# Kernel optimization log

Hardware: AMD Instinct MI355X
Metric: run time of the kernel (lower is better)

The kernel has to match this reference:

```python
import jax, jax.numpy as jnp
import numpy as np

B, T, D, L, H = 32, 256, 1024, 2, 8
DH = D // H          # 128 head dim
HID = 256            # GRU hidden per direction (d_model >> 1)
WIN = 3              # attn_width
NEG = -1e10


def setup_inputs() -> dict:
    key = jax.random.key(0)
    ks = jax.random.split(key, 20)
    s = 0.02
    inp = {}
    inp["x"] = jax.random.normal(ks[0], (B, T, 2560), jnp.float32)
    inp["mask"] = jnp.ones((B, T), jnp.int32)
    # face-feature projection Linear(1536, 512)
    inp["W_tran"] = jax.random.normal(ks[1], (1536, 512), jnp.float32) * s
    inp["b_tran"] = jnp.zeros((512,), jnp.float32)
    # stacked MHA params, one slice per layer
    inp["Wq"] = jax.random.normal(ks[2], (L, D, D), jnp.float32) * s
    inp["bq"] = jnp.zeros((L, D), jnp.float32)
    inp["Wk"] = jax.random.normal(ks[3], (L, D, D), jnp.float32) * s
    inp["bk"] = jnp.zeros((L, D), jnp.float32)
    inp["Wv"] = jax.random.normal(ks[4], (L, D, D), jnp.float32) * s
    inp["bv"] = jnp.zeros((L, D), jnp.float32)
    inp["Wo"] = jax.random.normal(ks[5], (L, D, D), jnp.float32) * s
    inp["bo"] = jnp.zeros((L, D), jnp.float32)
    # bidirectional GRU params (torch layout: [3H, in], gates r,z,n)
    inp["W_ih_f"] = jax.random.normal(ks[6], (3 * HID, D), jnp.float32) * s
    inp["W_hh_f"] = jax.random.normal(ks[7], (3 * HID, HID), jnp.float32) * s
    inp["b_ih_f"] = jnp.zeros((3 * HID,), jnp.float32)
    inp["b_hh_f"] = jnp.zeros((3 * HID,), jnp.float32)
    inp["W_ih_b"] = jax.random.normal(ks[8], (3 * HID, D), jnp.float32) * s
    inp["W_hh_b"] = jax.random.normal(ks[9], (3 * HID, HID), jnp.float32) * s
    inp["b_ih_b"] = jnp.zeros((3 * HID,), jnp.float32)
    inp["b_hh_b"] = jnp.zeros((3 * HID,), jnp.float32)
    return inp


def _gru(xs, W_ih, W_hh, b_ih, b_hh):
    # xs: [T, B, D] -> ys: [T, B, HID]
    gx = jnp.einsum('tbd,gd->tbg', xs, W_ih) + b_ih  # [T,B,3H]

    def step(h, g):
        gh = jnp.einsum('bh,gh->bg', h, W_hh) + b_hh
        r = jax.nn.sigmoid(g[:, :HID] + gh[:, :HID])
        z = jax.nn.sigmoid(g[:, HID:2 * HID] + gh[:, HID:2 * HID])
        n = jnp.tanh(g[:, 2 * HID:] + r * gh[:, 2 * HID:])
        h_new = (1.0 - z) * n + z * h
        return h_new, h_new

    h0 = jnp.zeros((xs.shape[1], HID), xs.dtype)
    _, ys = jax.lax.scan(step, h0, gx)
    return ys


def reference(x, mask, W_tran, b_tran, Wq, bq, Wk, bk, Wv, bv, Wo, bo,
              W_ih_f, W_hh_f, b_ih_f, b_hh_f, W_ih_b, W_hh_b, b_ih_b, b_hh_b):
    # split feature streams (Movie101 branch)
    x_face = jnp.einsum('btf,fd->btd', x[:, :, 1024:], W_tran) + b_tran  # [B,T,512]
    h = x[:, :, :1024]                                                   # [B,T,1024]

    # banded self-attn mask: 0 within |i-j|<=3, else -1e10
    idx = jnp.arange(T)
    band = jnp.where(jnp.abs(idx[:, None] - idx[None, :]) <= WIN, 0.0, NEG).astype(h.dtype)

    scale = 1.0 / np.sqrt(DH)
    for l in range(L):
        res = h
        q = (jnp.einsum('btd,de->bte', h, Wq[l]) + bq[l]).reshape(B, T, H, DH)
        k = (jnp.einsum('btd,de->bte', h, Wk[l]) + bk[l]).reshape(B, T, H, DH)
        v = (jnp.einsum('btd,de->bte', h, Wv[l]) + bv[l]).reshape(B, T, H, DH)
        scores = jnp.einsum('bqhd,bkhd->bhqk', q, k) * scale + band  # [B,H,T,T]
        attn = jax.nn.softmax(scores, axis=-1)
        out = jnp.einsum('bhqk,bkhd->bqhd', attn, v).reshape(B, T, D)
        out = jnp.einsum('btd,de->bte', out, Wo[l]) + bo[l]
        h = res + out  # dropout is identity in eval mode

    # BiGRU over time, respecting per-sequence lengths (packed semantics)
    xs = jnp.transpose(h, (1, 0, 2))                      # [T,B,1024]
    lengths = mask.sum(axis=-1)                           # [B]
    t_idx = jnp.arange(T)[:, None]                        # [T,1]
    valid = (t_idx < lengths[None, :]).astype(h.dtype)    # [T,B]

    ys_f = _gru(xs, W_ih_f, W_hh_f, b_ih_f, b_hh_f) * valid[:, :, None]

    # reverse each sequence within its own length
    rev_idx = jnp.clip(lengths[None, :] - 1 - t_idx, 0)   # [T,B]
    xs_rev = jnp.take_along_axis(xs, rev_idx[:, :, None], axis=0)
    ys_b = _gru(xs_rev, W_ih_b, W_hh_b, b_ih_b, b_hh_b)
    ys_b = jnp.take_along_axis(ys_b, rev_idx[:, :, None], axis=0) * valid[:, :, None]

    rnn_out = jnp.concatenate([ys_f, ys_b], axis=-1)      # [T,B,512]
    out = jnp.transpose(rnn_out, (1, 0, 2))               # [B,T,512]
    return out + x_face
```

## Files before the change

kernel.cpp:

```cpp
#include <hip/hip_runtime.h>
#include <hip/hip_fp16.h>

#define B_   32
#define T_   256
#define D_   1024
#define H_   8
#define HID_ 256

typedef unsigned short u16;
typedef __attribute__((ext_vector_type(8))) short  s16x8;
typedef __attribute__((ext_vector_type(8))) __bf16 bf16x8;
typedef __attribute__((ext_vector_type(4))) float  f32x4;
typedef __attribute__((ext_vector_type(2))) _Float16 h2v;
typedef __attribute__((ext_vector_type(8))) _Float16 h8;

__device__ __forceinline__ u16 f2bf(float f){
  union { float f; unsigned u; } v; v.f = f;
  unsigned r = v.u + 0x7FFFu + ((v.u >> 16) & 1u);
  return (u16)(r >> 16);
}
__device__ __forceinline__ float bf2f(u16 u){
  union { unsigned u; float f; } v; v.u = ((unsigned)u) << 16; return v.f;
}

__device__ __forceinline__ f32x4 mfma_bf16(s16x8 a, s16x8 b, f32x4 c){
  bf16x8 av, bv;
  __builtin_memcpy(&av, &a, 16);
  __builtin_memcpy(&bv, &b, 16);
  return __builtin_amdgcn_mfma_f32_16x16x32_bf16(av, bv, c, 0, 0, 0);
}

__device__ __forceinline__ void gld16(const void* g, void* l){
  __builtin_amdgcn_global_load_lds((const __attribute__((address_space(1))) void*)g,
                                   (__attribute__((address_space(3))) void*)l, 16, 0, 0);
}

#if defined(__has_builtin)
#if __has_builtin(__builtin_amdgcn_fdot2)
#define HAVE_FDOT2 1
#endif
#endif

__device__ __forceinline__ float fdot2f(h2v a, h2v b, float c){
#ifdef HAVE_FDOT2
  return __builtin_amdgcn_fdot2(a, b, c, false);
#else
  return c + (float)a[0]*(float)b[0] + (float)a[1]*(float)b[1];
#endif
}

__global__ void k_conv_x(const float* __restrict__ x, u16* __restrict__ h,
                         u16* __restrict__ xfb){
  int m = blockIdx.x;
  int i = threadIdx.x * 8;
  const float4* p = (const float4*)(x + (size_t)m*2560 + i);
  float4 a = p[0], b = p[1];
  union { u16 u[8]; uint4 v; } o;
  o.u[0]=f2bf(a.x); o.u[1]=f2bf(a.y); o.u[2]=f2bf(a.z); o.u[3]=f2bf(a.w);
  o.u[4]=f2bf(b.x); o.u[5]=f2bf(b.y); o.u[6]=f2bf(b.z); o.u[7]=f2bf(b.w);
  u16* dst = (i < 1024) ? (h + (size_t)m*1024 + i) : (xfb + (size_t)m*1536 + (i-1024));
  *(uint4*)dst = o.v;
}

__global__ void k_transpose_bf16(const float* __restrict__ in, u16* __restrict__ out,
                                 int K, int N){
  __shared__ u16 tile[64][65];
  int kb = blockIdx.y * 64, nb = blockIdx.x * 64;
  int tid = threadIdx.x;
  {
    int k  = tid >> 2;
    int n0 = (tid & 3) * 16;
    const float* ip = in + (size_t)(kb + k) * N + nb + n0;
    #pragma unroll
    for (int i = 0; i < 4; ++i){
      float4 v = *(const float4*)(ip + i*4);
      tile[k][n0 + i*4 + 0] = f2bf(v.x);
      tile[k][n0 + i*4 + 1] = f2bf(v.y);
      tile[k][n0 + i*4 + 2] = f2bf(v.z);
      tile[k][n0 + i*4 + 3] = f2bf(v.w);
    }
  }
  __syncthreads();
  {
    int n  = tid >> 2;
    int k0 = (tid & 3) * 16;
    union { u16 u[16]; uint4 v[2]; } p;
    #pragma unroll
    for (int i = 0; i < 16; ++i) p.u[i] = tile[k0 + i][n];
    uint4* op = (uint4*)(out + (size_t)(nb + n) * K + kb + k0);
    op[0] = p.v[0]; op[1] = p.v[1];
  }
}

__global__ void k_f32_to_bf16(const float* __restrict__ in, u16* __restrict__ out, int n){
  int i = blockIdx.x * blockDim.x + threadIdx.x;
  if (i < n) out[i] = f2bf(in[i]);
}
__global__ void k_f32_to_f16(const float* __restrict__ in, _Float16* __restrict__ out, int n){
  int i = blockIdx.x * blockDim.x + threadIdx.x;
  if (i < n) out[i] = (_Float16)in[i];
}
__global__ void k_copy_f32(const float* __restrict__ in, float* __restrict__ out, int n){
  int i = blockIdx.x * blockDim.x + threadIdx.x;
  if (i < n) out[i] = in[i];
}

__global__ void k_lengths(const int* __restrict__ mask, int* __restrict__ len){
  int b = blockIdx.x;
  int v = mask[b * T_ + threadIdx.x];
  #pragma unroll
  for (int off = 1; off < 64; off <<= 1) v += __shfl_xor(v, off);
  __shared__ int s[4];
  if ((threadIdx.x & 63) == 0) s[threadIdx.x >> 6] = v;
  __syncthreads();
  if (threadIdx.x == 0) len[b] = s[0] + s[1] + s[2] + s[3];
}

template<int MODE>
__global__ __launch_bounds__(256, 2)
void k_gemm(const u16* __restrict__ A, int lda,
            const u16* __restrict__ Wb,
            const float* __restrict__ bias,
            const void* __restrict__ resv,
            void* __restrict__ outv,
            int K, int N)
{
  __shared__ __align__(16) u16 As[4*128*8];
  __shared__ __align__(16) u16 Bs[4*128*8];
  int tid = threadIdx.x;
  int n0 = blockIdx.x * 128, m0 = blockIdx.y * 128;
  int lane = tid & 63, w = tid >> 6;
  int wm = w >> 1, wn = w & 1;
  int lrow = lane & 15, lq = lane >> 4;
  f32x4 acc[4][4] = {};

  int row = tid & 127;
  int kh0 = tid >> 7;
  const u16* aG0 = A  + (size_t)(m0 + row) * lda + kh0 * 8;
  const u16* bG0 = Wb + (size_t)(n0 + row) * K   + kh0 * 8;
  u16* aL0 = &As[((kh0    )*128 + row) * 8];
  u16* aL1 = &As[((kh0 + 2)*128 + row) * 8];
  u16* bL0 = &Bs[((kh0    )*128 + row) * 8];
  u16* bL1 = &Bs[((kh0 + 2)*128 + row) * 8];

  for (int k0 = 0; k0 < K; k0 += 32){
    gld16(aG0 + k0,      aL0);
    gld16(aG0 + k0 + 16, aL1);
    gld16(bG0 + k0,      bL0);
    gld16(bG0 + k0 + 16, bL1);
    __syncthreads();

    s16x8 af[4], bfr[4];
    #pragma unroll
    for (int mt = 0; mt < 4; ++mt)
      af[mt] = *(const s16x8*)&As[(lq*128 + wm*64 + mt*16 + lrow) * 8];
    #pragma unroll
    for (int nt = 0; nt < 4; ++nt)
      bfr[nt] = *(const s16x8*)&Bs[(lq*128 + wn*64 + nt*16 + lrow) * 8];
    #pragma unroll
    for (int mt = 0; mt < 4; ++mt)
      #pragma unroll
      for (int nt = 0; nt < 4; ++nt)
        acc[mt][nt] = mfma_bf16(af[mt], bfr[nt], acc[mt][nt]);
    __syncthreads();
  }

  #pragma unroll
  for (int mt = 0; mt < 4; ++mt){
    int rowb = m0 + wm*64 + mt*16 + lq*4;
    #pragma unroll
    for (int nt = 0; nt < 4; ++nt){
      int col = n0 + wn*64 + nt*16 + lrow;
      float bcol = bias[col];
      f32x4 a = acc[mt][nt];
      #pragma unroll
      for (int r = 0; r < 4; ++r){
        size_t idx = (size_t)(rowb + r) * N + col;
        float v = a[r] + bcol;
        if (MODE == 2) v += bf2f(((const u16*)resv)[idx]);
        if (MODE == 3) v += ((const float*)resv)[idx];
        if (MODE == 0 || MODE == 3) ((float*)outv)[idx] = v;
        else                        ((u16*)outv)[idx]   = f2bf(v);
      }
    }
  }
}

__global__ void k_attn(const u16* __restrict__ qkv, u16* __restrict__ ao){
  int lane = threadIdx.x & 63, wv = threadIdx.x >> 6;
  int bid = blockIdx.x;
  int t  = (bid & 63) * 4 + wv;
  int hh = (bid >> 6) & 7;
  int b  = bid >> 9;
  size_t qb = ((size_t)b*T_ + t)*3072 + hh*128 + lane*2;
  float2 q2;
  { ushort2 u = *(const ushort2*)(qkv + qb); q2.x = bf2f(u.x); q2.y = bf2f(u.y); }
  int jlo = t - 3; if (jlo < 0) jlo = 0;
  int jhi = t + 3; if (jhi > T_ - 1) jhi = T_ - 1;
  const float scale = 0.08838834764831845f;
  float m = -1e30f, sum = 0.f;
  float ox = 0.f, oy = 0.f;
  for (int j = jlo; j <= jhi; ++j){
    size_t kb = ((size_t)b*T_ + j)*3072 + 1024 + hh*128 + lane*2;
    float2 k2, v2;
    { ushort2 u = *(const ushort2*)(qkv + kb);        k2.x = bf2f(u.x); k2.y = bf2f(u.y); }
    { ushort2 u = *(const ushort2*)(qkv + kb + 1024); v2.x = bf2f(u.x); v2.y = bf2f(u.y); }
    float s = q2.x*k2.x + q2.y*k2.y;
    s += __shfl_xor(s, 1);  s += __shfl_xor(s, 2);  s += __shfl_xor(s, 4);
    s += __shfl_xor(s, 8);  s += __shfl_xor(s, 16); s += __shfl_xor(s, 32);
    float f  = s * scale;
    float nm = fmaxf(m, f);
    float c  = __expf(m - nm);
    float p  = __expf(f - nm);
    sum = sum*c + p;
    ox = ox*c + p*v2.x;
    oy = oy*c + p*v2.y;
    m = nm;
  }
  float inv = 1.f / sum;
  size_t ob = ((size_t)b*T_ + t)*1024 + hh*128 + lane*2;
  ushort2 r; r.x = f2bf(ox*inv); r.y = f2bf(oy*inv);
  *(ushort2*)(ao + ob) = r;
}

__global__ __launch_bounds__(1024, 4)
void k_gru(const _Float16* __restrict__ WhhF, const _Float16* __restrict__ WhhB,
           const float* __restrict__ bhhF, const float* __restrict__ bhhB,
           const float* __restrict__ gx,
           const int* __restrict__ lengths, float* __restrict__ out)
{
  int dir = blockIdx.x >> 5, b = blockIdx.x & 31;
  const _Float16* Whh = dir ? WhhB : WhhF;
  const float*    bhh = dir ? bhhB : bhhF;
  int tid = threadIdx.x;
  int j = tid >> 2, kc = tid & 3;

  h8 wgt[3][8];
  #pragma unroll
  for (int g = 0; g < 3; ++g)
    #pragma unroll
    for (int c = 0; c < 8; ++c)
      wgt[g][c] = *(const h8*)(Whh + (size_t)(g*256 + j)*256 + (c*4 + kc)*8);
  float bb0 = bhh[j], bb1 = bhh[256 + j], bb2 = bhh[512 + j];

  __shared__ __align__(16) _Float16 hc[2][256];
  if (tid < 256) hc[0][tid] = (_Float16)0.f;
  int len = lengths[b];
  if (tid < 256){
    for (int t = len; t < T_; ++t)
      out[((size_t)b*T_ + t)*512 + dir*256 + tid] = 0.f;
  }
  float hprev = 0.f;
  float gR = 0.f, gZ = 0.f, gN = 0.f;
  if (kc == 0 && len > 0){
    int tt0 = dir ? (len - 1) : 0;
    size_t gb = ((size_t)b*T_ + tt0)*1536 + dir*768 + j;
    gR = gx[gb]; gZ = gx[gb + 256]; gN = gx[gb + 512];
  }
  __syncthreads();

  for (int s = 0; s < len; ++s){
    float nR = 0.f, nZ = 0.f, nN = 0.f;
    if (kc == 0 && s + 1 < len){
      int tn = dir ? (len - 2 - s) : (s + 1);
      size_t gb = ((size_t)b*T_ + tn)*1536 + dir*768 + j;
      nR = gx[gb]; nZ = gx[gb + 256]; nN = gx[gb + 512];
    }
    const _Float16* hbuf = hc[s & 1];
    float aR = 0.f, aZ = 0.f, aN = 0.f;
    #pragma unroll
    for (int c = 0; c < 8; ++c){
      h8 hv = *(const h8*)(hbuf + (c*4 + kc)*8);
      h8 w0v = wgt[0][c], w1v = wgt[1][c], w2v = wgt[2][c];
#define GRU_DOT(i) {                                                          \
      h2v hp = __builtin_shufflevector(hv, hv, 2*(i), 2*(i)+1);               \
      aR = fdot2f(__builtin_shufflevector(w0v, w0v, 2*(i), 2*(i)+1), hp, aR); \
      aZ = fdot2f(__builtin_shufflevector(w1v, w1v, 2*(i), 2*(i)+1), hp, aZ); \
      aN = fdot2f(__builtin_shufflevector(w2v, w2v, 2*(i), 2*(i)+1), hp, aN); }
      GRU_DOT(0) GRU_DOT(1) GRU_DOT(2) GRU_DOT(3)
#undef GRU_DOT
    }
    aR += __shfl_xor(aR, 1); aR += __shfl_xor(aR, 2);
    aZ += __shfl_xor(aZ, 1); aZ += __shfl_xor(aZ, 2);
    aN += __shfl_xor(aN, 1); aN += __shfl_xor(aN, 2);
    if (kc == 0){
      int tt = dir ? (len - 1 - s) : s;
      float r = 1.f / (1.f + __expf(-(gR + aR + bb0)));
      float z = 1.f / (1.f + __expf(-(gZ + aZ + bb1)));
      float e = __expf(2.f*(gN + r*(aN + bb2)));
      float n = 1.f - 2.f/(e + 1.f);
      float hnew = (1.f - z)*n + z*hprev;
      hprev = hnew;
      out[((size_t)b*T_ + tt)*512 + dir*256 + j] = hnew;
      hc[(s + 1) & 1][j] = (_Float16)hnew;
    }
    gR = nR; gZ = nZ; gN = nN;
    __syncthreads();
  }
}

extern "C" void kernel_launch(void* const* d_in, const int* in_sizes, int n_in,
                              void* d_out, int out_size, void* d_ws, size_t ws_size,
                              hipStream_t stream)
{
  const float* x     = (const float*)d_in[0];
  const int*   mask  = (const int*)  d_in[1];
  const float* Wtran = (const float*)d_in[2];
  const float* btran = (const float*)d_in[3];
  const float* Wq    = (const float*)d_in[4];
  const float* bq    = (const float*)d_in[5];
  const float* Wk    = (const float*)d_in[6];
  const float* bk    = (const float*)d_in[7];
  const float* Wv    = (const float*)d_in[8];
  const float* bv    = (const float*)d_in[9];
  const float* Wo    = (const float*)d_in[10];
  const float* bo    = (const float*)d_in[11];
  const float* Wihf  = (const float*)d_in[12];
  const float* Whhf  = (const float*)d_in[13];
  const float* bihf  = (const float*)d_in[14];
  const float* bhhf  = (const float*)d_in[15];
  const float* Wihb  = (const float*)d_in[16];
  const float* Whhb  = (const float*)d_in[17];
  const float* bihb  = (const float*)d_in[18];
  const float* bhhb  = (const float*)d_in[19];
  float* out = (float*)d_out;

  char* ws = (char*)d_ws;
  const size_t MT = (size_t)B_ * T_;
  u16* h      = (u16*)(ws);
  u16* xfb    = (u16*)(ws + 16777216);
  u16* ao     = (u16*)(ws + 41943040);
  u16* qkv    = (u16*)(ws + 58720256);
  float* gx   = (float*)qkv;
  u16* WtranT = (u16*)(ws + 109051904);
  u16* WqkvT  = (u16*)(ws + 110624768);
  u16* WoT    = (u16*)(ws + 123207680);
  u16* WihCat = (u16*)(ws + 127401984);
  _Float16* WhhFh = (_Float16*)(ws + 130547712);
  _Float16* WhhBh = WhhFh + (size_t)768*256;
  float* qkvB  = (float*)(ws + 131334144);
  float* bihCat= (float*)(ws + 131358720);
  int* lens    = (int*)(ws + 131364864);

  k_conv_x<<<8192, 320, 0, stream>>>(x, h, xfb);
  k_transpose_bf16<<<dim3(8, 24), 256, 0, stream>>>(Wtran, WtranT, 1536, 512);
  for (int l = 0; l < 2; ++l){
    size_t wo = (size_t)l * D_ * D_;
    size_t qo = (size_t)l * 3 * D_ * D_;
    k_transpose_bf16<<<dim3(16,16), 256, 0, stream>>>(Wq + wo, WqkvT + qo,               D_, D_);
    k_transpose_bf16<<<dim3(16,16), 256, 0, stream>>>(Wk + wo, WqkvT + qo + (size_t)D_*D_,   D_, D_);
    k_transpose_bf16<<<dim3(16,16), 256, 0, stream>>>(Wv + wo, WqkvT + qo + (size_t)2*D_*D_, D_, D_);
    k_transpose_bf16<<<dim3(16,16), 256, 0, stream>>>(Wo + wo, WoT + wo, D_, D_);
    k_copy_f32<<<4, 256, 0, stream>>>(bq + l*D_, qkvB + l*3072,        D_);
    k_copy_f32<<<4, 256, 0, stream>>>(bk + l*D_, qkvB + l*3072 + 1024, D_);
    k_copy_f32<<<4, 256, 0, stream>>>(bv + l*D_, qkvB + l*3072 + 2048, D_);
  }
  {
    int n = 768*1024;
    k_f32_to_bf16<<<(n+255)/256, 256, 0, stream>>>(Wihf, WihCat, n);
    k_f32_to_bf16<<<(n+255)/256, 256, 0, stream>>>(Wihb, WihCat + (size_t)768*1024, n);
    int m = 768*256;
    k_f32_to_f16<<<(m+255)/256, 256, 0, stream>>>(Whhf, WhhFh, m);
    k_f32_to_f16<<<(m+255)/256, 256, 0, stream>>>(Whhb, WhhBh, m);
    k_copy_f32<<<3, 256, 0, stream>>>(bihf, bihCat,       768);
    k_copy_f32<<<3, 256, 0, stream>>>(bihb, bihCat + 768, 768);
  }
  k_lengths<<<32, 256, 0, stream>>>(mask, lens);

  for (int l = 0; l < 2; ++l){
    size_t qo = (size_t)l * 3 * D_ * D_;
    size_t wo = (size_t)l * D_ * D_;
    k_gemm<1><<<dim3(24,64), 256, 0, stream>>>(h, D_, WqkvT + qo, qkvB + l*3072,
                                               nullptr, qkv, D_, 3072);
    k_attn<<<16384, 256, 0, stream>>>(qkv, ao);
    k_gemm<2><<<dim3(8,64), 256, 0, stream>>>(ao, D_, WoT + wo, bo + l*D_,
                                              h, h, D_, D_);
  }

  k_gemm<0><<<dim3(12,64), 256, 0, stream>>>(h, D_, WihCat, bihCat,
                                             nullptr, gx, D_, 1536);
  k_gru<<<64, 1024, 0, stream>>>(WhhFh, WhhBh, bhhf, bhhb, gx, lens, out);

  k_gemm<3><<<dim3(4,64), 256, 0, stream>>>(xfb, 1536, WtranT, btran,
                                            out, out, 1536, 512);
}
```

Baseline: 1.099 ms.

## Double GEMM K-step to 64 and halve GRU threads with more weights per thread

The GEMM kernel now stages a 64-wide K slice per iteration in twice the LDS. This halves the number of barrier pairs and gives each wave twice as many MFMAs between syncs. The GRU kernel uses 512 threads per block, so each thread holds 16 chunks of recurrent weights per gate in registers, and the cross-lane reduction drops from two shuffles to one. The risk is higher VGPR pressure in the GRU, handled with an asm barrier that pins the weights in registers, plus longer serial dot products per step.

```diff
diff --git a/kernel.cpp b/kernel.cpp
--- a/kernel.cpp
+++ b/kernel.cpp
@@ -125,8 +125,8 @@
             void* __restrict__ outv,
             int K, int N)
 {
-  __shared__ __align__(16) u16 As[4*128*8];
-  __shared__ __align__(16) u16 Bs[4*128*8];
+  __shared__ __align__(16) u16 As[8*128*8];
+  __shared__ __align__(16) u16 Bs[8*128*8];
   int tid = threadIdx.x;
   int n0 = blockIdx.x * 128, m0 = blockIdx.y * 128;
   int lane = tid & 63, w = tid >> 6;
@@ -136,32 +136,40 @@
 
   int row = tid & 127;
   int kh0 = tid >> 7;
-  const u16* aG0 = A  + (size_t)(m0 + row) * lda + kh0 * 8;
-  const u16* bG0 = Wb + (size_t)(n0 + row) * K   + kh0 * 8;
-  u16* aL0 = &As[((kh0    )*128 + row) * 8];
-  u16* aL1 = &As[((kh0 + 2)*128 + row) * 8];
-  u16* bL0 = &Bs[((kh0    )*128 + row) * 8];
-  u16* bL1 = &Bs[((kh0 + 2)*128 + row) * 8];
-
-  for (int k0 = 0; k0 < K; k0 += 32){
-    gld16(aG0 + k0,      aL0);
-    gld16(aG0 + k0 + 16, aL1);
-    gld16(bG0 + k0,      bL0);
-    gld16(bG0 + k0 + 16, bL1);
+  const u16* aG = A  + (size_t)(m0 + row) * lda + kh0 * 8;
+  const u16* bG = Wb + (size_t)(n0 + row) * K   + kh0 * 8;
+  u16* aL[4]; u16* bL[4];
+  #pragma unroll
+  for (int c = 0; c < 4; ++c){
+    aL[c] = &As[((kh0 + 2*c)*128 + row) * 8];
+    bL[c] = &Bs[((kh0 + 2*c)*128 + row) * 8];
+  }
+
+  for (int k0 = 0; k0 < K; k0 += 64){
+    #pragma unroll
+    for (int c = 0; c < 4; ++c){
+      gld16(aG + k0 + c*16, aL[c]);
+      gld16(bG + k0 + c*16, bL[c]);
+    }
     __syncthreads();
 
-    s16x8 af[4], bfr[4];
-    #pragma unroll
-    for (int mt = 0; mt < 4; ++mt)
-      af[mt] = *(const s16x8*)&As[(lq*128 + wm*64 + mt*16 + lrow) * 8];
-    #pragma unroll
-    for (int nt = 0; nt < 4; ++nt)
-      bfr[nt] = *(const s16x8*)&Bs[(lq*128 + wn*64 + nt*16 + lrow) * 8];
-    #pragma unroll
-    for (int mt = 0; mt < 4; ++mt)
+    s16x8 af[2][4], bfr[2][4];
+    #pragma unroll
+    for (int ks = 0; ks < 2; ++ks){
+      #pragma unroll
+      for (int mt = 0; mt < 4; ++mt)
+        af[ks][mt] = *(const s16x8*)&As[((ks*4 + lq)*128 + wm*64 + mt*16 + lrow) * 8];
       #pragma unroll
       for (int nt = 0; nt < 4; ++nt)
-        acc[mt][nt] = mfma_bf16(af[mt], bfr[nt], acc[mt][nt]);
+        bfr[ks][nt] = *(const s16x8*)&Bs[((ks*4 + lq)*128 + wn*64 + nt*16 + lrow) * 8];
+    }
+    #pragma unroll
+    for (int ks = 0; ks < 2; ++ks)
+      #pragma unroll
+      for (int mt = 0; mt < 4; ++mt)
+        #pragma unroll
+        for (int nt = 0; nt < 4; ++nt)
+          acc[mt][nt] = mfma_bf16(af[ks][mt], bfr[ks][nt], acc[mt][nt]);
     __syncthreads();
   }
 
@@ -223,7 +231,7 @@
   *(ushort2*)(ao + ob) = r;
 }
 
-__global__ __launch_bounds__(1024, 4)
+__global__ __launch_bounds__(512, 2)
 void k_gru(const _Float16* __restrict__ WhhF, const _Float16* __restrict__ WhhB,
            const float* __restrict__ bhhF, const float* __restrict__ bhhB,
            const float* __restrict__ gx,
@@ -233,14 +241,19 @@
   const _Float16* Whh = dir ? WhhB : WhhF;
   const float*    bhh = dir ? bhhB : bhhF;
   int tid = threadIdx.x;
-  int j = tid >> 2, kc = tid & 3;
-
-  h8 wgt[3][8];
+  int j = tid >> 1, kc = tid & 1;
+
+  h8 wgt[3][16];
   #pragma unroll
   for (int g = 0; g < 3; ++g)
     #pragma unroll
-    for (int c = 0; c < 8; ++c)
-      wgt[g][c] = *(const h8*)(Whh + (size_t)(g*256 + j)*256 + (c*4 + kc)*8);
+    for (int c = 0; c < 16; ++c)
+      wgt[g][c] = *(const h8*)(Whh + (size_t)(g*256 + j)*256 + (c*2 + kc)*8);
+  #pragma unroll
+  for (int g = 0; g < 3; ++g)
+    #pragma unroll
+    for (int c = 0; c < 16; ++c)
+      asm volatile("" : "+v"(wgt[g][c]));
   float bb0 = bhh[j], bb1 = bhh[256 + j], bb2 = bhh[512 + j];
 
   __shared__ __align__(16) _Float16 hc[2][256];
@@ -269,8 +282,8 @@
     const _Float16* hbuf = hc[s & 1];
     float aR = 0.f, aZ = 0.f, aN = 0.f;
     #pragma unroll
-    for (int c = 0; c < 8; ++c){
-      h8 hv = *(const h8*)(hbuf + (c*4 + kc)*8);
+    for (int c = 0; c < 16; ++c){
+      h8 hv = *(const h8*)(hbuf + (c*2 + kc)*8);
       h8 w0v = wgt[0][c], w1v = wgt[1][c], w2v = wgt[2][c];
 #define GRU_DOT(i) {                                                          \
       h2v hp = __builtin_shufflevector(hv, hv, 2*(i), 2*(i)+1);               \
@@ -280,9 +293,9 @@
       GRU_DOT(0) GRU_DOT(1) GRU_DOT(2) GRU_DOT(3)
 #undef GRU_DOT
     }
-    aR += __shfl_xor(aR, 1); aR += __shfl_xor(aR, 2);
-    aZ += __shfl_xor(aZ, 1); aZ += __shfl_xor(aZ, 2);
-    aN += __shfl_xor(aN, 1); aN += __shfl_xor(aN, 2);
+    aR += __shfl_xor(aR, 1);
+    aZ += __shfl_xor(aZ, 1);
+    aN += __shfl_xor(aN, 1);
     if (kc == 0){
       int tt = dir ? (len - 1 - s) : s;
       float r = 1.f / (1.f + __expf(-(gR + aR + bb0)));
@@ -379,7 +392,7 @@
 
   k_gemm<0><<<dim3(12,64), 256, 0, stream>>>(h, D_, WihCat, bihCat,
                                              nullptr, gx, D_, 1536);
-  k_gru<<<64, 1024, 0, stream>>>(WhhFh, WhhBh, bhhf, bhhb, gx, lens, out);
+  k_gru<<<64, 512, 0, stream>>>(WhhFh, WhhBh, bhhf, bhhb, gx, lens, out);
 
   k_gemm<3><<<dim3(4,64), 256, 0, stream>>>(xfb, 1536, WtranT, btran,
                                             out, out, 1536, 512);
```

Result: no change. 1.080 ms (-1.8%).

## Quantize GRU recurrent weights to FP8 and fuse weight-prep kernels into one launch

Applied to the files above, without the earlier changes.

The recurrent GRU weights are now stored as FP8 (scaled by 64) in a per-thread packed layout. They are decoded to fp16 pairs inside the step loop, which halves the register footprint of the weights (48 ints instead of 96) so the 1024-thread block fits the waves-per-EU target without spilling. All weight transposes, conversions, bias copies and the length reduction are merged into a single k_prep launch, removing many small kernel launches. The cost is lower precision in the recurrent matmul and extra decode instructions on the serial critical path.

```diff
diff --git a/kernel.cpp b/kernel.cpp
--- a/kernel.cpp
+++ b/kernel.cpp
@@ -11,6 +11,7 @@
 typedef __attribute__((ext_vector_type(8))) short  s16x8;
 typedef __attribute__((ext_vector_type(8))) __bf16 bf16x8;
 typedef __attribute__((ext_vector_type(4))) float  f32x4;
+typedef __attribute__((ext_vector_type(2))) float  f32x2;
 typedef __attribute__((ext_vector_type(2))) _Float16 h2v;
 typedef __attribute__((ext_vector_type(8))) _Float16 h8;
 
@@ -47,6 +48,19 @@
 #else
   return c + (float)a[0]*(float)b[0] + (float)a[1]*(float)b[1];
 #endif
+}
+
+__device__ __forceinline__ h2v dec2(short s){
+  h2v r;
+#if defined(__has_builtin) && __has_builtin(__builtin_amdgcn_cvt_pk_f16_fp8)
+  auto p = __builtin_amdgcn_cvt_pk_f16_fp8(s);
+  __builtin_memcpy(&r, &p, 4);
+#else
+  f32x2 f = __builtin_amdgcn_cvt_pk_f32_fp8((int)(unsigned short)s, false);
+  auto p = __builtin_amdgcn_cvt_pkrtz(f[0], f[1]);
+  __builtin_memcpy(&r, &p, 4);
+#endif
+  return r;
 }
 
 __global__ void k_conv_x(const float* __restrict__ x, u16* __restrict__ h,
@@ -62,11 +76,9 @@
   *(uint4*)dst = o.v;
 }
 
-__global__ void k_transpose_bf16(const float* __restrict__ in, u16* __restrict__ out,
-                                 int K, int N){
-  __shared__ u16 tile[64][65];
-  int kb = blockIdx.y * 64, nb = blockIdx.x * 64;
-  int tid = threadIdx.x;
+__device__ void transpose_tile(const float* __restrict__ in, u16* __restrict__ out,
+                               int K, int N, int kb, int nb, int tid,
+                               u16 (*tile)[65]){
   {
     int k  = tid >> 2;
     int n0 = (tid & 3) * 16;
@@ -92,28 +104,84 @@
   }
 }
 
-__global__ void k_f32_to_bf16(const float* __restrict__ in, u16* __restrict__ out, int n){
-  int i = blockIdx.x * blockDim.x + threadIdx.x;
-  if (i < n) out[i] = f2bf(in[i]);
-}
-__global__ void k_f32_to_f16(const float* __restrict__ in, _Float16* __restrict__ out, int n){
-  int i = blockIdx.x * blockDim.x + threadIdx.x;
-  if (i < n) out[i] = (_Float16)in[i];
-}
-__global__ void k_copy_f32(const float* __restrict__ in, float* __restrict__ out, int n){
-  int i = blockIdx.x * blockDim.x + threadIdx.x;
-  if (i < n) out[i] = in[i];
-}
-
-__global__ void k_lengths(const int* __restrict__ mask, int* __restrict__ len){
-  int b = blockIdx.x;
-  int v = mask[b * T_ + threadIdx.x];
-  #pragma unroll
-  for (int off = 1; off < 64; off <<= 1) v += __shfl_xor(v, off);
-  __shared__ int s[4];
-  if ((threadIdx.x & 63) == 0) s[threadIdx.x >> 6] = v;
-  __syncthreads();
-  if (threadIdx.x == 0) len[b] = s[0] + s[1] + s[2] + s[3];
+__global__ void k_prep(const float* __restrict__ Wq, const float* __restrict__ Wk,
+                       const float* __restrict__ Wv, const float* __restrict__ Wo,
+                       const float* __restrict__ Wtran,
+                       const float* __restrict__ Wihf, const float* __restrict__ Wihb,
+                       const float* __restrict__ Whhf, const float* __restrict__ Whhb,
+                       const float* __restrict__ bq, const float* __restrict__ bk,
+                       const float* __restrict__ bv,
+                       const float* __restrict__ bihf, const float* __restrict__ bihb,
+                       const int* __restrict__ mask,
+                       u16* __restrict__ WqkvT, u16* __restrict__ WoT,
+                       u16* __restrict__ WtranT, u16* __restrict__ WihCat,
+                       int* __restrict__ Wp, float* __restrict__ qkvB,
+                       float* __restrict__ bihCat, int* __restrict__ lens)
+{
+  __shared__ u16 tile[64][65];
+  int bid = blockIdx.x, tid = threadIdx.x;
+  const size_t M1 = (size_t)D_ * D_;
+
+  if (bid < 2048){
+    int m = bid >> 8, t = bid & 255;
+    int l = m >> 2, which = m & 3;
+    const float* src; u16* dst;
+    if (which == 0){ src = Wq + l*M1; dst = WqkvT + l*3*M1; }
+    else if (which == 1){ src = Wk + l*M1; dst = WqkvT + l*3*M1 + M1; }
+    else if (which == 2){ src = Wv + l*M1; dst = WqkvT + l*3*M1 + 2*M1; }
+    else { src = Wo + l*M1; dst = WoT + l*M1; }
+    transpose_tile(src, dst, D_, D_, (t >> 4)*64, (t & 15)*64, tid, tile);
+  } else if (bid < 2240){
+    int t = bid - 2048;
+    transpose_tile(Wtran, WtranT, 1536, 512, (t >> 3)*64, (t & 7)*64, tid, tile);
+  } else if (bid < 3008){
+    int i0 = (bid - 2240)*2048 + tid*8;
+    const float* src = (i0 < 786432) ? (Wihf + i0) : (Wihb + (i0 - 786432));
+    float4 a = *(const float4*)src, b = *(const float4*)(src + 4);
+    union { u16 u[8]; uint4 v; } o;
+    o.u[0]=f2bf(a.x); o.u[1]=f2bf(a.y); o.u[2]=f2bf(a.z); o.u[3]=f2bf(a.w);
+    o.u[4]=f2bf(b.x); o.u[5]=f2bf(b.y); o.u[6]=f2bf(b.z); o.u[7]=f2bf(b.w);
+    *(uint4*)(WihCat + i0) = o.v;
+  } else if (bid < 3392){
+    int o = (bid - 3008)*256 + tid;
+    int dir = o / 49152, r = o - dir*49152;
+    int tid2 = r / 48, q = r - tid2*48;
+    int g = q >> 4, c = (q & 15) >> 1, di = q & 1;
+    int j = tid2 >> 2, kc = tid2 & 3;
+    int row = g*256 + j;
+    int k0 = (c*4 + kc)*8 + di*4;
+    const float* W = dir ? Whhb : Whhf;
+    const float* wsrc = W + (size_t)row*256 + k0;
+    int d = __builtin_amdgcn_cvt_pk_fp8_f32(wsrc[0]*64.f, wsrc[1]*64.f, 0, false);
+    d     = __builtin_amdgcn_cvt_pk_fp8_f32(wsrc[2]*64.f, wsrc[3]*64.f, d, true);
+    Wp[o] = d;
+  } else if (bid < 3400){
+    int base = (bid - 3392)*1024 + tid*4;
+    #pragma unroll
+    for (int e = 0; e < 4; ++e){
+      int i = base + e;
+      if (i >= 7680) break;
+      if (i < 6144){
+        int l = i / 3072, r = i - l*3072;
+        float v = (r < 1024) ? bq[l*1024 + r]
+                : (r < 2048) ? bk[l*1024 + r - 1024]
+                             : bv[l*1024 + r - 2048];
+        qkvB[i] = v;
+      } else {
+        int r = i - 6144;
+        bihCat[r] = (r < 768) ? bihf[r] : bihb[r - 768];
+      }
+    }
+  } else {
+    int b = bid - 3400;
+    int v = mask[b * T_ + tid];
+    #pragma unroll
+    for (int off = 1; off < 64; off <<= 1) v += __shfl_xor(v, off);
+    __shared__ int s[4];
+    if ((tid & 63) == 0) s[tid >> 6] = v;
+    __syncthreads();
+    if (tid == 0) lens[b] = s[0] + s[1] + s[2] + s[3];
+  }
 }
 
 template<int MODE>
@@ -223,24 +291,29 @@
   *(ushort2*)(ao + ob) = r;
 }
 
-__global__ __launch_bounds__(1024, 4)
-void k_gru(const _Float16* __restrict__ WhhF, const _Float16* __restrict__ WhhB,
+__global__ __attribute__((amdgpu_flat_work_group_size(1024,1024), amdgpu_waves_per_eu(4,4)))
+void k_gru(const int* __restrict__ Wp,
            const float* __restrict__ bhhF, const float* __restrict__ bhhB,
            const float* __restrict__ gx,
            const int* __restrict__ lengths, float* __restrict__ out)
 {
   int dir = blockIdx.x >> 5, b = blockIdx.x & 31;
-  const _Float16* Whh = dir ? WhhB : WhhF;
-  const float*    bhh = dir ? bhhB : bhhF;
+  const float* bhh = dir ? bhhB : bhhF;
   int tid = threadIdx.x;
   int j = tid >> 2, kc = tid & 3;
 
-  h8 wgt[3][8];
+  int wv[48];
+  {
+    const uint4* wp4 = (const uint4*)(Wp + (size_t)dir*49152 + (size_t)tid*48);
+    #pragma unroll
+    for (int c = 0; c < 12; ++c){
+      uint4 t4 = wp4[c];
+      wv[c*4+0]=(int)t4.x; wv[c*4+1]=(int)t4.y; wv[c*4+2]=(int)t4.z; wv[c*4+3]=(int)t4.w;
+    }
+  }
   #pragma unroll
-  for (int g = 0; g < 3; ++g)
-    #pragma unroll
-    for (int c = 0; c < 8; ++c)
-      wgt[g][c] = *(const h8*)(Whh + (size_t)(g*256 + j)*256 + (c*4 + kc)*8);
+  for (int i = 0; i < 48; ++i) asm volatile("" : "+v"(wv[i]));
+
   float bb0 = bhh[j], bb1 = bhh[256 + j], bb2 = bhh[512 + j];
 
   __shared__ __align__(16) _Float16 hc[2][256];
@@ -271,23 +344,24 @@
     #pragma unroll
     for (int c = 0; c < 8; ++c){
       h8 hv = *(const h8*)(hbuf + (c*4 + kc)*8);
-      h8 w0v = wgt[0][c], w1v = wgt[1][c], w2v = wgt[2][c];
-#define GRU_DOT(i) {                                                          \
-      h2v hp = __builtin_shufflevector(hv, hv, 2*(i), 2*(i)+1);               \
-      aR = fdot2f(__builtin_shufflevector(w0v, w0v, 2*(i), 2*(i)+1), hp, aR); \
-      aZ = fdot2f(__builtin_shufflevector(w1v, w1v, 2*(i), 2*(i)+1), hp, aZ); \
-      aN = fdot2f(__builtin_shufflevector(w2v, w2v, 2*(i), 2*(i)+1), hp, aN); }
-      GRU_DOT(0) GRU_DOT(1) GRU_DOT(2) GRU_DOT(3)
-#undef GRU_DOT
+      h2v hp0 = (h2v){hv[0], hv[1]}, hp1 = (h2v){hv[2], hv[3]},
+          hp2 = (h2v){hv[4], hv[5]}, hp3 = (h2v){hv[6], hv[7]};
+#define GATE(g, AC) { int lo = wv[(g)*16 + c*2], hi = wv[(g)*16 + c*2 + 1];   \
+      AC = fdot2f(dec2((short)(lo & 0xffff)), hp0, AC);                        \
+      AC = fdot2f(dec2((short)(((unsigned)lo) >> 16)), hp1, AC);               \
+      AC = fdot2f(dec2((short)(hi & 0xffff)), hp2, AC);                        \
+      AC = fdot2f(dec2((short)(((unsigned)hi) >> 16)), hp3, AC); }
+      GATE(0, aR) GATE(1, aZ) GATE(2, aN)
+#undef GATE
     }
     aR += __shfl_xor(aR, 1); aR += __shfl_xor(aR, 2);
     aZ += __shfl_xor(aZ, 1); aZ += __shfl_xor(aZ, 2);
     aN += __shfl_xor(aN, 1); aN += __shfl_xor(aN, 2);
     if (kc == 0){
       int tt = dir ? (len - 1 - s) : s;
-      float r = 1.f / (1.f + __expf(-(gR + aR + bb0)));
-      float z = 1.f / (1.f + __expf(-(gZ + aZ + bb1)));
-      float e = __expf(2.f*(gN + r*(aN + bb2)));
+      float r = 1.f / (1.f + __expf(-(gR + aR*0.015625f + bb0)));
+      float z = 1.f / (1.f + __expf(-(gZ + aZ*0.015625f + bb1)));
+      float e = __expf(2.f*(gN + r*(aN*0.015625f + bb2)));
       float n = 1.f - 2.f/(e + 1.f);
       float hnew = (1.f - z)*n + z*hprev;
       hprev = hnew;
@@ -326,7 +400,6 @@
   float* out = (float*)d_out;
 
   char* ws = (char*)d_ws;
-  const size_t MT = (size_t)B_ * T_;
   u16* h      = (u16*)(ws);
   u16* xfb    = (u16*)(ws + 16777216);
   u16* ao     = (u16*)(ws + 41943040);
@@ -336,36 +409,15 @@
   u16* WqkvT  = (u16*)(ws + 110624768);
   u16* WoT    = (u16*)(ws + 123207680);
   u16* WihCat = (u16*)(ws + 127401984);
-  _Float16* WhhFh = (_Float16*)(ws + 130547712);
-  _Float16* WhhBh = WhhFh + (size_t)768*256;
+  int* Wp     = (int*)(ws + 130547712);
   float* qkvB  = (float*)(ws + 131334144);
   float* bihCat= (float*)(ws + 131358720);
   int* lens    = (int*)(ws + 131364864);
 
+  k_prep<<<3432, 256, 0, stream>>>(Wq, Wk, Wv, Wo, Wtran, Wihf, Wihb, Whhf, Whhb,
+                                   bq, bk, bv, bihf, bihb, mask,
+                                   WqkvT, WoT, WtranT, WihCat, Wp, qkvB, bihCat, lens);
   k_conv_x<<<8192, 320, 0, stream>>>(x, h, xfb);
-  k_transpose_bf16<<<dim3(8, 24), 256, 0, stream>>>(Wtran, WtranT, 1536, 512);
-  for (int l = 0; l < 2; ++l){
-    size_t wo = (size_t)l * D_ * D_;
-    size_t qo = (size_t)l * 3 * D_ * D_;
-    k_transpose_bf16<<<dim3(16,16), 256, 0, stream>>>(Wq + wo, WqkvT + qo,               D_, D_);
-    k_transpose_bf16<<<dim3(16,16), 256, 0, stream>>>(Wk + wo, WqkvT + qo + (size_t)D_*D_,   D_, D_);
-    k_transpose_bf16<<<dim3(16,16), 256, 0, stream>>>(Wv + wo, WqkvT + qo + (size_t)2*D_*D_, D_, D_);
-    k_transpose_bf16<<<dim3(16,16), 256, 0, stream>>>(Wo + wo, WoT + wo, D_, D_);
-    k_copy_f32<<<4, 256, 0, stream>>>(bq + l*D_, qkvB + l*3072,        D_);
-    k_copy_f32<<<4, 256, 0, stream>>>(bk + l*D_, qkvB + l*3072 + 1024, D_);
-    k_copy_f32<<<4, 256, 0, stream>>>(bv + l*D_, qkvB + l*3072 + 2048, D_);
-  }
-  {
-    int n = 768*1024;
-    k_f32_to_bf16<<<(n+255)/256, 256, 0, stream>>>(Wihf, WihCat, n);
-    k_f32_to_bf16<<<(n+255)/256, 256, 0, stream>>>(Wihb, WihCat + (size_t)768*1024, n);
-    int m = 768*256;
-    k_f32_to_f16<<<(m+255)/256, 256, 0, stream>>>(Whhf, WhhFh, m);
-    k_f32_to_f16<<<(m+255)/256, 256, 0, stream>>>(Whhb, WhhBh, m);
-    k_copy_f32<<<3, 256, 0, stream>>>(bihf, bihCat,       768);
-    k_copy_f32<<<3, 256, 0, stream>>>(bihb, bihCat + 768, 768);
-  }
-  k_lengths<<<32, 256, 0, stream>>>(mask, lens);
 
   for (int l = 0; l < 2; ++l){
     size_t qo = (size_t)l * 3 * D_ * D_;
@@ -379,7 +431,7 @@
 
   k_gemm<0><<<dim3(12,64), 256, 0, stream>>>(h, D_, WihCat, bihCat,
                                              nullptr, gx, D_, 1536);
-  k_gru<<<64, 1024, 0, stream>>>(WhhFh, WhhBh, bhhf, bhhb, gx, lens, out);
+  k_gru<<<64, 1024, 0, stream>>>(Wp, bhhf, bhhb, gx, lens, out);
 
   k_gemm<3><<<dim3(4,64), 256, 0, stream>>>(xfb, 1536, WtranT, btran,
                                             out, out, 1536, 512);
```

Result: faster. 1.077 ms (-2.1%).
